# Kernel optimization log

Measured on AMD Instinct MI355X. Metric: run time of the kernel, lower is better.

## Reference

```python
import jax, jax.numpy as jnp
import numpy as np

B, IN, H = 4096, 2048, 2048

def hard_sigmoid(x):
    # torch nn.Hardsigmoid / QHardSigmoid: clip(x/6 + 0.5, 0, 1)
    return jnp.clip(x / 6.0 + 0.5, 0.0, 1.0)

def hard_tanh(x):
    return jnp.clip(x, -1.0, 1.0)

def setup_inputs() -> dict:
    key = jax.random.key(0)
    k1, k2, k3, k4, k5 = jax.random.split(key, 5)
    return {
        "input_": jax.random.normal(k1, (B, IN), dtype=jnp.float32),
        "h_0": jax.random.normal(k2, (B, H), dtype=jnp.float32),
        "c_0": jax.random.normal(k3, (B, H), dtype=jnp.float32),
        "W_ih": jax.random.normal(k4, (4 * H, IN), dtype=jnp.float32) * (1.0 / np.sqrt(IN)),
        "W_hh": jax.random.normal(k5, (4 * H, H), dtype=jnp.float32) * (1.0 / np.sqrt(H)),
        "b_hh": jnp.zeros((4 * H,), dtype=jnp.float32),
    }

def reference(input_, h_0, c_0, W_ih, W_hh, b_hh):
    # Two GEMMs: x @ W_ih^T (no bias) and h @ W_hh^T + b
    wi = jnp.einsum('bi,gi->bg', input_, W_ih)          # [B, 4H]
    wh_b = jnp.einsum('bh,gh->bg', h_0, W_hh) + b_hh     # [B, 4H]
    h_x4 = wh_b + wi
    f, i, o, g = jnp.split(h_x4, 4, axis=1)              # split order: f, i, o, g
    new = hard_sigmoid(i) * hard_tanh(g)
    old = hard_sigmoid(f) * c_0
    c_1 = old + new
    h_1 = hard_sigmoid(o) * hard_tanh(c_1)
    return (h_1, c_1)
```

## Files before the change

### kernel.cpp

```cpp
#include <hip/hip_runtime.h>
#include <hip/hip_bf16.h>


typedef __attribute__((ext_vector_type(8))) short short8;
typedef __attribute__((ext_vector_type(4))) float f32x4;

#define B_SZ 4096
#define K_SZ 4096
#define N_SZ 8192
#define H_SZ 2048

typedef const __attribute__((address_space(1))) void gvoid_t;
typedef __attribute__((address_space(3))) void lvoid_t;

__device__ __forceinline__ void gload_lds16(const __hip_bfloat16* g, void* l) {
    __builtin_amdgcn_global_load_lds((gvoid_t*)g, (lvoid_t*)l, 16, 0, 0);
}

__device__ __forceinline__ float hsig(float x) {
    return fminf(fmaxf(x * (1.0f / 6.0f) + 0.5f, 0.0f), 1.0f);
}
__device__ __forceinline__ float htanh(float x) {
    return fminf(fmaxf(x, -1.0f), 1.0f);
}

__device__ __forceinline__ void cvt8_store(const float* src, __hip_bfloat16* dst) {
    float4 v0 = *reinterpret_cast<const float4*>(src);
    float4 v1 = *reinterpret_cast<const float4*>(src + 4);
    union { __hip_bfloat16 h[8]; uint4 q; } p;
    p.h[0] = __float2bfloat16(v0.x); p.h[1] = __float2bfloat16(v0.y);
    p.h[2] = __float2bfloat16(v0.z); p.h[3] = __float2bfloat16(v0.w);
    p.h[4] = __float2bfloat16(v1.x); p.h[5] = __float2bfloat16(v1.y);
    p.h[6] = __float2bfloat16(v1.z); p.h[7] = __float2bfloat16(v1.w);
    *reinterpret_cast<uint4*>(dst) = p.q;
}

__global__ void cvt_concat_kernel(const float* __restrict__ a,
                                  const float* __restrict__ b,
                                  __hip_bfloat16* __restrict__ out,
                                  int total8)
{
    int i = blockIdx.x * blockDim.x + threadIdx.x;
    if (i >= total8) return;
    int idx = i << 3;
    int r = idx >> 12;
    int c = idx & 4095;
    const float* src = (c < 2048) ? (a + (size_t)r * 2048 + c)
                                  : (b + (size_t)r * 2048 + (c - 2048));
    cvt8_store(src, out + idx);
}

__global__ void cvt_w_perm_kernel(const float* __restrict__ wih,
                                  const float* __restrict__ whh,
                                  __hip_bfloat16* __restrict__ out,
                                  int total8)
{
    int i = blockIdx.x * blockDim.x + threadIdx.x;
    if (i >= total8) return;
    int idx = i << 3;
    int r = idx >> 12;
    int c = idx & 4095;
    int gate = (((r >> 7) & 1) << 1) | ((r >> 4) & 1);
    int j = (r & 15) | (((r >> 5) & 3) << 4) | ((r >> 8) << 6);
    int srow = gate * 2048 + j;
    const float* src = (c < 2048) ? (wih + (size_t)srow * 2048 + c)
                                  : (whh + (size_t)srow * 2048 + (c - 2048));
    cvt8_store(src, out + idx);
}

__global__ __launch_bounds__(512, 2)
void gemm_fused_kernel(const __hip_bfloat16* __restrict__ A,
                       const __hip_bfloat16* __restrict__ Bw,
                       const float* __restrict__ c0,
                       const float* __restrict__ bias,
                       float* __restrict__ out)
{
    constexpr int BK = 64;
    constexpr int NT = K_SZ / BK;
    constexpr int NWG = (B_SZ / 256) * (N_SZ / 256);
    constexpr int TILEB = 65536;

    extern __shared__ __align__(16) char lds[];

    const int tid  = threadIdx.x;
    const int wave = tid >> 6;
    const int lane = tid & 63;
    const int wrow = wave >> 2;
    const int wcol = wave & 3;
    const int fr   = lane & 15;
    const int fkq  = lane >> 4;

    int bid = blockIdx.x;
    int swz = (bid & 7) * (NWG / 8) + (bid >> 3);
    int bm = swz >> 5;
    int bn = swz & 31;

    const int rs  = tid >> 3;
    const int ch  = tid & 7;
    const int lch = ch ^ (rs & 7);
    const __hip_bfloat16* pa = A  + (size_t)(bm * 256 + rs) * K_SZ + lch * 8;
    const __hip_bfloat16* pb = Bw + (size_t)(bn * 256 + rs) * K_SZ + lch * 8;

#define STG_A(bufn, kt, srow) \
    gload_lds16(pa + (size_t)(srow) * K_SZ + (kt), (bufn) + (srow) * 128 + wave * 1024)
#define STG_B(bufn, kt, srow) \
    gload_lds16(pb + (size_t)(srow) * K_SZ + (kt), (bufn) + 32768 + (srow) * 128 + wave * 1024)

    int a_off[4], b_off[2];
#pragma unroll
    for (int mf = 0; mf < 4; ++mf) {
        int row = wrow * 64 + mf * 16 + fr;
        a_off[mf] = row * 128 + ((fkq ^ (row & 7)) << 4);
    }
#pragma unroll
    for (int nf = 0; nf < 2; ++nf) {
        int row = wcol * 32 + nf * 16 + fr;
        b_off[nf] = row * 128 + ((fkq ^ (row & 7)) << 4);
    }

    f32x4 acc[8][4];
#pragma unroll
    for (int m = 0; m < 8; ++m)
#pragma unroll
        for (int n = 0; n < 4; ++n)
            acc[m][n] = f32x4{0.f, 0.f, 0.f, 0.f};

    {
        char* b0 = lds;
        STG_A(b0, 0, 0);   STG_A(b0, 0, 64);
        STG_B(b0, 0, 0);   STG_B(b0, 0, 64);
        STG_B(b0, 0, 128); STG_B(b0, 0, 192);
        STG_A(b0, 0, 128); STG_A(b0, 0, 192);
    }
    asm volatile("s_waitcnt vmcnt(2)" ::: "memory");
    asm volatile("s_barrier" ::: "memory");

    short8 av[4][2], bv0[2][2], bv1[2][2];

#pragma unroll 1
    for (int t = 0; t < NT; ++t) {
        char* bufc = lds + (t & 1) * TILEB;
        char* bufn = lds + ((t + 1) & 1) * TILEB;
        const char* Ab = bufc;
        const char* Bb = bufc + 32768;
        const int ktn = (t + 1) * BK;
        const bool st = (t + 1 < NT);

#pragma unroll
        for (int mf = 0; mf < 4; ++mf)
#pragma unroll
            for (int ks = 0; ks < 2; ++ks)
                av[mf][ks] = *(const short8*)(Ab + (a_off[mf] ^ (ks << 6)));
#pragma unroll
        for (int nf = 0; nf < 2; ++nf)
#pragma unroll
            for (int ks = 0; ks < 2; ++ks) {
                bv0[nf][ks] = *(const short8*)(Bb + (b_off[nf] ^ (ks << 6)));
                bv1[nf][ks] = *(const short8*)(Bb + 16384 + (b_off[nf] ^ (ks << 6)));
            }
        if (st) { STG_A(bufn, ktn, 0); STG_A(bufn, ktn, 64); }
        asm volatile("s_barrier" ::: "memory");
        asm volatile("s_waitcnt lgkmcnt(0)" ::: "memory");
        __builtin_amdgcn_sched_barrier(0);
        __builtin_amdgcn_s_setprio(1);
#pragma unroll
        for (int mf = 0; mf < 4; ++mf)
#pragma unroll
            for (int nf = 0; nf < 2; ++nf)
#pragma unroll
                for (int ks = 0; ks < 2; ++ks)
                    acc[mf][nf] = __builtin_amdgcn_mfma_f32_16x16x32_bf16(av[mf][ks], bv0[nf][ks], acc[mf][nf], 0, 0, 0);
        __builtin_amdgcn_s_setprio(0);
        asm volatile("s_barrier" ::: "memory");

        if (st) { STG_B(bufn, ktn, 0); STG_B(bufn, ktn, 64); }
        asm volatile("s_barrier" ::: "memory");
        __builtin_amdgcn_s_setprio(1);
#pragma unroll
        for (int mf = 0; mf < 4; ++mf)
#pragma unroll
            for (int nf = 0; nf < 2; ++nf)
#pragma unroll
                for (int ks = 0; ks < 2; ++ks)
                    acc[mf][2 + nf] = __builtin_amdgcn_mfma_f32_16x16x32_bf16(av[mf][ks], bv1[nf][ks], acc[mf][2 + nf], 0, 0, 0);
        __builtin_amdgcn_s_setprio(0);
        if (st) asm volatile("s_waitcnt vmcnt(4)" ::: "memory");
        else    asm volatile("s_waitcnt vmcnt(0)" ::: "memory");
        asm volatile("s_barrier" ::: "memory");

#pragma unroll
        for (int mf = 0; mf < 4; ++mf)
#pragma unroll
            for (int ks = 0; ks < 2; ++ks)
                av[mf][ks] = *(const short8*)(Ab + 16384 + (a_off[mf] ^ (ks << 6)));
        if (st) { STG_B(bufn, ktn, 128); STG_B(bufn, ktn, 192); }
        asm volatile("s_barrier" ::: "memory");
        asm volatile("s_waitcnt lgkmcnt(0)" ::: "memory");
        __builtin_amdgcn_sched_barrier(0);
        __builtin_amdgcn_s_setprio(1);
#pragma unroll
        for (int mf = 0; mf < 4; ++mf)
#pragma unroll
            for (int nf = 0; nf < 2; ++nf)
#pragma unroll
                for (int ks = 0; ks < 2; ++ks)
                    acc[4 + mf][nf] = __builtin_amdgcn_mfma_f32_16x16x32_bf16(av[mf][ks], bv0[nf][ks], acc[4 + mf][nf], 0, 0, 0);
        __builtin_amdgcn_s_setprio(0);
        asm volatile("s_barrier" ::: "memory");

        if (st) { STG_A(bufn, ktn, 128); STG_A(bufn, ktn, 192); }
        asm volatile("s_barrier" ::: "memory");
        __builtin_amdgcn_s_setprio(1);
#pragma unroll
        for (int mf = 0; mf < 4; ++mf)
#pragma unroll
            for (int nf = 0; nf < 2; ++nf)
#pragma unroll
                for (int ks = 0; ks < 2; ++ks)
                    acc[4 + mf][2 + nf] = __builtin_amdgcn_mfma_f32_16x16x32_bf16(av[mf][ks], bv1[nf][ks], acc[4 + mf][2 + nf], 0, 0, 0);
        __builtin_amdgcn_s_setprio(0);
        if (st) asm volatile("s_waitcnt vmcnt(2)" ::: "memory");
        asm volatile("s_barrier" ::: "memory");
    }
#undef STG_A
#undef STG_B

    const int jj = bn * 64 + wcol * 16 + fr;
    const float bf = bias[jj];
    const float bi = bias[2048 + jj];
    const float bo = bias[4096 + jj];
    const float bg = bias[6144 + jj];
    float* h1out = out;
    float* c1out = out + (size_t)B_SZ * H_SZ;
#pragma unroll
    for (int mh = 0; mh < 2; ++mh)
#pragma unroll
        for (int mf = 0; mf < 4; ++mf) {
            const int m = mh * 4 + mf;
            const int row0 = bm * 256 + mh * 128 + wrow * 64 + mf * 16 + fkq * 4;
#pragma unroll
            for (int i = 0; i < 4; ++i) {
                int r = row0 + i;
                float c0v = c0[(size_t)r * H_SZ + jj];
                float f  = acc[m][0][i] + bf;
                float ig = acc[m][1][i] + bi;
                float o  = acc[m][2][i] + bo;
                float g  = acc[m][3][i] + bg;
                float cn = hsig(f) * c0v + hsig(ig) * htanh(g);
                h1out[(size_t)r * H_SZ + jj] = hsig(o) * htanh(cn);
                c1out[(size_t)r * H_SZ + jj] = cn;
            }
        }
}

extern "C" void kernel_launch(void* const* d_in, const int* in_sizes, int n_in,
                              void* d_out, int out_size, void* d_ws, size_t ws_size,
                              hipStream_t stream)
{
    const float* x   = (const float*)d_in[0];
    const float* h0  = (const float*)d_in[1];
    const float* c0  = (const float*)d_in[2];
    const float* Wih = (const float*)d_in[3];
    const float* Whh = (const float*)d_in[4];
    const float* bhh = (const float*)d_in[5];
    float* out = (float*)d_out;

    if (ws_size < (size_t)96 * 1024 * 1024) return;
    char* ws = (char*)d_ws;
    __hip_bfloat16* Xp = (__hip_bfloat16*)ws;
    __hip_bfloat16* Wp = (__hip_bfloat16*)(ws + (size_t)32 * 1024 * 1024);

    int t8x = B_SZ * K_SZ / 8;
    cvt_concat_kernel<<<t8x / 256, 256, 0, stream>>>(x, h0, Xp, t8x);
    int t8w = N_SZ * K_SZ / 8;
    cvt_w_perm_kernel<<<t8w / 256, 256, 0, stream>>>(Wih, Whh, Wp, t8w);

    gemm_fused_kernel<<<512, 512, 131072, stream>>>(Xp, Wp, c0, bhh, out);
}
```

Before: 467.2 us.

## Fuse fp32-to-bf16 conversion and weight permutation into GEMM tile loads

Removes the two separate conversion kernels and the bf16 workspace. The GEMM now loads fp32 activations and weights straight from global memory into registers, packs them to bf16 and writes them into the swizzled LDS layout, computing the gate permutation inline. It also merges the two MFMA half-phases per A sub-tile and drops several barriers. The intent is to avoid extra launches and the round trip through the workspace. The cost is twice the global bytes per tile (fp32 instead of bf16), conversion work repeated by every tile that reuses the same data, more register pressure, and no longer using direct global-to-LDS loads.

```diff
diff --git a/kernel.cpp b/kernel.cpp
--- a/kernel.cpp
+++ b/kernel.cpp
@@ -10,13 +10,6 @@
 #define N_SZ 8192
 #define H_SZ 2048
 
-typedef const __attribute__((address_space(1))) void gvoid_t;
-typedef __attribute__((address_space(3))) void lvoid_t;
-
-__device__ __forceinline__ void gload_lds16(const __hip_bfloat16* g, void* l) {
-    __builtin_amdgcn_global_load_lds((gvoid_t*)g, (lvoid_t*)l, 16, 0, 0);
-}
-
 __device__ __forceinline__ float hsig(float x) {
     return fminf(fmaxf(x * (1.0f / 6.0f) + 0.5f, 0.0f), 1.0f);
 }
@@ -24,53 +17,20 @@
     return fminf(fmaxf(x, -1.0f), 1.0f);
 }
 
-__device__ __forceinline__ void cvt8_store(const float* src, __hip_bfloat16* dst) {
-    float4 v0 = *reinterpret_cast<const float4*>(src);
-    float4 v1 = *reinterpret_cast<const float4*>(src + 4);
+__device__ __forceinline__ uint4 pack8(float4 lo, float4 hi) {
     union { __hip_bfloat16 h[8]; uint4 q; } p;
-    p.h[0] = __float2bfloat16(v0.x); p.h[1] = __float2bfloat16(v0.y);
-    p.h[2] = __float2bfloat16(v0.z); p.h[3] = __float2bfloat16(v0.w);
-    p.h[4] = __float2bfloat16(v1.x); p.h[5] = __float2bfloat16(v1.y);
-    p.h[6] = __float2bfloat16(v1.z); p.h[7] = __float2bfloat16(v1.w);
-    *reinterpret_cast<uint4*>(dst) = p.q;
-}
-
-__global__ void cvt_concat_kernel(const float* __restrict__ a,
-                                  const float* __restrict__ b,
-                                  __hip_bfloat16* __restrict__ out,
-                                  int total8)
-{
-    int i = blockIdx.x * blockDim.x + threadIdx.x;
-    if (i >= total8) return;
-    int idx = i << 3;
-    int r = idx >> 12;
-    int c = idx & 4095;
-    const float* src = (c < 2048) ? (a + (size_t)r * 2048 + c)
-                                  : (b + (size_t)r * 2048 + (c - 2048));
-    cvt8_store(src, out + idx);
-}
-
-__global__ void cvt_w_perm_kernel(const float* __restrict__ wih,
-                                  const float* __restrict__ whh,
-                                  __hip_bfloat16* __restrict__ out,
-                                  int total8)
-{
-    int i = blockIdx.x * blockDim.x + threadIdx.x;
-    if (i >= total8) return;
-    int idx = i << 3;
-    int r = idx >> 12;
-    int c = idx & 4095;
-    int gate = (((r >> 7) & 1) << 1) | ((r >> 4) & 1);
-    int j = (r & 15) | (((r >> 5) & 3) << 4) | ((r >> 8) << 6);
-    int srow = gate * 2048 + j;
-    const float* src = (c < 2048) ? (wih + (size_t)srow * 2048 + c)
-                                  : (whh + (size_t)srow * 2048 + (c - 2048));
-    cvt8_store(src, out + idx);
+    p.h[0] = __float2bfloat16(lo.x); p.h[1] = __float2bfloat16(lo.y);
+    p.h[2] = __float2bfloat16(lo.z); p.h[3] = __float2bfloat16(lo.w);
+    p.h[4] = __float2bfloat16(hi.x); p.h[5] = __float2bfloat16(hi.y);
+    p.h[6] = __float2bfloat16(hi.z); p.h[7] = __float2bfloat16(hi.w);
+    return p.q;
 }
 
 __global__ __launch_bounds__(512, 2)
-void gemm_fused_kernel(const __hip_bfloat16* __restrict__ A,
-                       const __hip_bfloat16* __restrict__ Bw,
+void gemm_fused_kernel(const float* __restrict__ x,
+                       const float* __restrict__ h0,
+                       const float* __restrict__ wih,
+                       const float* __restrict__ whh,
                        const float* __restrict__ c0,
                        const float* __restrict__ bias,
                        float* __restrict__ out)
@@ -95,16 +55,18 @@
     int bm = swz >> 5;
     int bn = swz & 31;
 
-    const int rs  = tid >> 3;
-    const int ch  = tid & 7;
-    const int lch = ch ^ (rs & 7);
-    const __hip_bfloat16* pa = A  + (size_t)(bm * 256 + rs) * K_SZ + lch * 8;
-    const __hip_bfloat16* pb = Bw + (size_t)(bn * 256 + rs) * K_SZ + lch * 8;
-
-#define STG_A(bufn, kt, srow) \
-    gload_lds16(pa + (size_t)(srow) * K_SZ + (kt), (bufn) + (srow) * 128 + wave * 1024)
-#define STG_B(bufn, kt, srow) \
-    gload_lds16(pb + (size_t)(srow) * K_SZ + (kt), (bufn) + 32768 + (srow) * 128 + wave * 1024)
+    const int rs = tid >> 3;
+    const int ch = tid & 7;
+    const int abase = (bm * 256 + rs) * 2048 + ch * 8;
+    int boff[4];
+#pragma unroll
+    for (int k = 0; k < 4; ++k) {
+        int br = rs + k * 64;
+        int gate = (((br >> 7) & 1) << 1) | ((br >> 4) & 1);
+        int j = (br & 15) | (((br >> 5) & 3) << 4) | (bn << 6);
+        boff[k] = (gate * 2048 + j) * 2048 + ch * 8;
+    }
+    const int adst = rs * 128 + ((ch ^ (rs & 7)) << 4);
 
     int a_off[4], b_off[2];
 #pragma unroll
@@ -125,17 +87,42 @@
         for (int n = 0; n < 4; ++n)
             acc[m][n] = f32x4{0.f, 0.f, 0.f, 0.f};
 
+    float4 aL0, aH0, aL1, aH1;
+    float4 bL0, bH0, bL1, bH1;
+
+#define LD_A(k0) { \
+    const float* p0 = As + abase + (k0) * 131072 + kc; \
+    const float* p1 = As + abase + ((k0) + 1) * 131072 + kc; \
+    aL0 = *(const float4*)(p0); aH0 = *(const float4*)(p0 + 4); \
+    aL1 = *(const float4*)(p1); aH1 = *(const float4*)(p1 + 4); }
+#define LD_B(k0) { \
+    const float* p0 = Ws + boff[k0] + kc; \
+    const float* p1 = Ws + boff[(k0) + 1] + kc; \
+    bL0 = *(const float4*)(p0); bH0 = *(const float4*)(p0 + 4); \
+    bL1 = *(const float4*)(p1); bH1 = *(const float4*)(p1 + 4); }
+#define WR_A(k0) { \
+    *(uint4*)(bufn + adst + (k0) * 8192) = pack8(aL0, aH0); \
+    *(uint4*)(bufn + adst + ((k0) + 1) * 8192) = pack8(aL1, aH1); }
+#define WR_B(k0) { \
+    *(uint4*)(bufn + 32768 + adst + (k0) * 8192) = pack8(bL0, bH0); \
+    *(uint4*)(bufn + 32768 + adst + ((k0) + 1) * 8192) = pack8(bL1, bH1); }
+
     {
-        char* b0 = lds;
-        STG_A(b0, 0, 0);   STG_A(b0, 0, 64);
-        STG_B(b0, 0, 0);   STG_B(b0, 0, 64);
-        STG_B(b0, 0, 128); STG_B(b0, 0, 192);
-        STG_A(b0, 0, 128); STG_A(b0, 0, 192);
-    }
-    asm volatile("s_waitcnt vmcnt(2)" ::: "memory");
-    asm volatile("s_barrier" ::: "memory");
-
-    short8 av[4][2], bv0[2][2], bv1[2][2];
+        char* bufn = lds;
+        const float* As = x;
+        const float* Ws = wih;
+        const int kc = 0;
+        LD_A(0); LD_B(0);
+        asm volatile("s_waitcnt vmcnt(4)" ::: "memory");
+        WR_A(0); LD_A(2);
+        asm volatile("s_waitcnt vmcnt(4)" ::: "memory");
+        WR_B(0); LD_B(2);
+        asm volatile("s_waitcnt vmcnt(4)" ::: "memory");
+        WR_A(2);
+        asm volatile("s_waitcnt vmcnt(0)" ::: "memory");
+        WR_B(2);
+        asm volatile("s_waitcnt lgkmcnt(0)" ::: "memory");
+    }
 
 #pragma unroll 1
     for (int t = 0; t < NT; ++t) {
@@ -143,9 +130,18 @@
         char* bufn = lds + ((t + 1) & 1) * TILEB;
         const char* Ab = bufc;
         const char* Bb = bufc + 32768;
-        const int ktn = (t + 1) * BK;
         const bool st = (t + 1 < NT);
-
+        const int knext = (t + 1) * BK;
+        const bool inx = knext < 2048;
+        const float* As = inx ? x : h0;
+        const float* Ws = inx ? wih : whh;
+        const int kc = knext & 2047;
+
+        asm volatile("s_barrier" ::: "memory");
+
+        if (st) { LD_A(0); LD_B(0); }
+
+        short8 av[4][2], bv0[2][2], bv1[2][2];
 #pragma unroll
         for (int mf = 0; mf < 4; ++mf)
 #pragma unroll
@@ -158,8 +154,6 @@
                 bv0[nf][ks] = *(const short8*)(Bb + (b_off[nf] ^ (ks << 6)));
                 bv1[nf][ks] = *(const short8*)(Bb + 16384 + (b_off[nf] ^ (ks << 6)));
             }
-        if (st) { STG_A(bufn, ktn, 0); STG_A(bufn, ktn, 64); }
-        asm volatile("s_barrier" ::: "memory");
         asm volatile("s_waitcnt lgkmcnt(0)" ::: "memory");
         __builtin_amdgcn_sched_barrier(0);
         __builtin_amdgcn_s_setprio(1);
@@ -168,33 +162,27 @@
 #pragma unroll
             for (int nf = 0; nf < 2; ++nf)
 #pragma unroll
-                for (int ks = 0; ks < 2; ++ks)
-                    acc[mf][nf] = __builtin_amdgcn_mfma_f32_16x16x32_bf16(av[mf][ks], bv0[nf][ks], acc[mf][nf], 0, 0, 0);
+                for (int ks = 0; ks < 2; ++ks) {
+                    acc[mf][nf]     = __builtin_amdgcn_mfma_f32_16x16x32_bf16(av[mf][ks], bv0[nf][ks], acc[mf][nf], 0, 0, 0);
+                    acc[mf][2 + nf] = __builtin_amdgcn_mfma_f32_16x16x32_bf16(av[mf][ks], bv1[nf][ks], acc[mf][2 + nf], 0, 0, 0);
+                }
         __builtin_amdgcn_s_setprio(0);
-        asm volatile("s_barrier" ::: "memory");
-
-        if (st) { STG_B(bufn, ktn, 0); STG_B(bufn, ktn, 64); }
-        asm volatile("s_barrier" ::: "memory");
-        __builtin_amdgcn_s_setprio(1);
-#pragma unroll
-        for (int mf = 0; mf < 4; ++mf)
-#pragma unroll
-            for (int nf = 0; nf < 2; ++nf)
-#pragma unroll
-                for (int ks = 0; ks < 2; ++ks)
-                    acc[mf][2 + nf] = __builtin_amdgcn_mfma_f32_16x16x32_bf16(av[mf][ks], bv1[nf][ks], acc[mf][2 + nf], 0, 0, 0);
-        __builtin_amdgcn_s_setprio(0);
-        if (st) asm volatile("s_waitcnt vmcnt(4)" ::: "memory");
-        else    asm volatile("s_waitcnt vmcnt(0)" ::: "memory");
-        asm volatile("s_barrier" ::: "memory");
-
+
+        if (st) {
+            asm volatile("s_waitcnt vmcnt(4)" ::: "memory");
+            __builtin_amdgcn_sched_barrier(0);
+            WR_A(0); LD_A(2);
+            asm volatile("s_waitcnt vmcnt(4)" ::: "memory");
+            __builtin_amdgcn_sched_barrier(0);
+            WR_B(0); LD_B(2);
+        }
+
+        short8 aw[4][2];
 #pragma unroll
         for (int mf = 0; mf < 4; ++mf)
 #pragma unroll
             for (int ks = 0; ks < 2; ++ks)
-                av[mf][ks] = *(const short8*)(Ab + 16384 + (a_off[mf] ^ (ks << 6)));
-        if (st) { STG_B(bufn, ktn, 128); STG_B(bufn, ktn, 192); }
-        asm volatile("s_barrier" ::: "memory");
+                aw[mf][ks] = *(const short8*)(Ab + 16384 + (a_off[mf] ^ (ks << 6)));
         asm volatile("s_waitcnt lgkmcnt(0)" ::: "memory");
         __builtin_amdgcn_sched_barrier(0);
         __builtin_amdgcn_s_setprio(1);
@@ -203,27 +191,26 @@
 #pragma unroll
             for (int nf = 0; nf < 2; ++nf)
 #pragma unroll
-                for (int ks = 0; ks < 2; ++ks)
-                    acc[4 + mf][nf] = __builtin_amdgcn_mfma_f32_16x16x32_bf16(av[mf][ks], bv0[nf][ks], acc[4 + mf][nf], 0, 0, 0);
+                for (int ks = 0; ks < 2; ++ks) {
+                    acc[4 + mf][nf]     = __builtin_amdgcn_mfma_f32_16x16x32_bf16(aw[mf][ks], bv0[nf][ks], acc[4 + mf][nf], 0, 0, 0);
+                    acc[4 + mf][2 + nf] = __builtin_amdgcn_mfma_f32_16x16x32_bf16(aw[mf][ks], bv1[nf][ks], acc[4 + mf][2 + nf], 0, 0, 0);
+                }
         __builtin_amdgcn_s_setprio(0);
-        asm volatile("s_barrier" ::: "memory");
-
-        if (st) { STG_A(bufn, ktn, 128); STG_A(bufn, ktn, 192); }
-        asm volatile("s_barrier" ::: "memory");
-        __builtin_amdgcn_s_setprio(1);
-#pragma unroll
-        for (int mf = 0; mf < 4; ++mf)
-#pragma unroll
-            for (int nf = 0; nf < 2; ++nf)
-#pragma unroll
-                for (int ks = 0; ks < 2; ++ks)
-                    acc[4 + mf][2 + nf] = __builtin_amdgcn_mfma_f32_16x16x32_bf16(av[mf][ks], bv1[nf][ks], acc[4 + mf][2 + nf], 0, 0, 0);
-        __builtin_amdgcn_s_setprio(0);
-        if (st) asm volatile("s_waitcnt vmcnt(2)" ::: "memory");
-        asm volatile("s_barrier" ::: "memory");
-    }
-#undef STG_A
-#undef STG_B
+
+        if (st) {
+            asm volatile("s_waitcnt vmcnt(4)" ::: "memory");
+            __builtin_amdgcn_sched_barrier(0);
+            WR_A(2);
+            asm volatile("s_waitcnt vmcnt(0)" ::: "memory");
+            __builtin_amdgcn_sched_barrier(0);
+            WR_B(2);
+            asm volatile("s_waitcnt lgkmcnt(0)" ::: "memory");
+        }
+    }
+#undef LD_A
+#undef LD_B
+#undef WR_A
+#undef WR_B
 
     const int jj = bn * 64 + wcol * 16 + fr;
     const float bf = bias[jj];
@@ -265,15 +252,5 @@
     const float* bhh = (const float*)d_in[5];
     float* out = (float*)d_out;
 
-    if (ws_size < (size_t)96 * 1024 * 1024) return;
-    char* ws = (char*)d_ws;
-    __hip_bfloat16* Xp = (__hip_bfloat16*)ws;
-    __hip_bfloat16* Wp = (__hip_bfloat16*)(ws + (size_t)32 * 1024 * 1024);
-
-    int t8x = B_SZ * K_SZ / 8;
-    cvt_concat_kernel<<<t8x / 256, 256, 0, stream>>>(x, h0, Xp, t8x);
-    int t8w = N_SZ * K_SZ / 8;
-    cvt_w_perm_kernel<<<t8w / 256, 256, 0, stream>>>(Wih, Whh, Wp, t8w);
-
-    gemm_fused_kernel<<<512, 512, 131072, stream>>>(Xp, Wp, c0, bhh, out);
-}
+    gemm_fused_kernel<<<512, 512, 131072, stream>>>(x, h0, Wih, Whh, c0, bhh, out);
+}
```

New measurement: 1.071 ms. 129% more time.

## Merge conversion kernels and restructure GEMM main loop into two phases

Applied to the files above, without the earlier changes.

Combines the two fp32-to-bf16 conversion kernels into a single grid-stride launch, removing one kernel launch. The GEMM main loop goes from four barrier-separated MFMA phases with interleaved partial tile loads to two phases. All eight global-to-LDS loads for the next tile are issued up front, and each phase now covers both B halves. This cuts the number of barriers per K-step and lengthens MFMA runs, but it issues all prefetches at once and adds an extra A register set, which may raise register pressure at 2 waves/SIMD occupancy.

```diff
diff --git a/kernel.cpp b/kernel.cpp
--- a/kernel.cpp
+++ b/kernel.cpp
@@ -35,37 +35,36 @@
     *reinterpret_cast<uint4*>(dst) = p.q;
 }
 
-__global__ void cvt_concat_kernel(const float* __restrict__ a,
-                                  const float* __restrict__ b,
-                                  __hip_bfloat16* __restrict__ out,
-                                  int total8)
+__global__ void cvt_all_kernel(const float* __restrict__ x,
+                               const float* __restrict__ h0,
+                               const float* __restrict__ wih,
+                               const float* __restrict__ whh,
+                               __hip_bfloat16* __restrict__ Xp,
+                               __hip_bfloat16* __restrict__ Wp)
 {
-    int i = blockIdx.x * blockDim.x + threadIdx.x;
-    if (i >= total8) return;
-    int idx = i << 3;
-    int r = idx >> 12;
-    int c = idx & 4095;
-    const float* src = (c < 2048) ? (a + (size_t)r * 2048 + c)
-                                  : (b + (size_t)r * 2048 + (c - 2048));
-    cvt8_store(src, out + idx);
-}
-
-__global__ void cvt_w_perm_kernel(const float* __restrict__ wih,
-                                  const float* __restrict__ whh,
-                                  __hip_bfloat16* __restrict__ out,
-                                  int total8)
-{
-    int i = blockIdx.x * blockDim.x + threadIdx.x;
-    if (i >= total8) return;
-    int idx = i << 3;
-    int r = idx >> 12;
-    int c = idx & 4095;
-    int gate = (((r >> 7) & 1) << 1) | ((r >> 4) & 1);
-    int j = (r & 15) | (((r >> 5) & 3) << 4) | ((r >> 8) << 6);
-    int srow = gate * 2048 + j;
-    const float* src = (c < 2048) ? (wih + (size_t)srow * 2048 + c)
-                                  : (whh + (size_t)srow * 2048 + (c - 2048));
-    cvt8_store(src, out + idx);
+    constexpr int XT = B_SZ * K_SZ / 8;
+    constexpr int WT = N_SZ * K_SZ / 8;
+    const int stride = gridDim.x * blockDim.x;
+    for (int i = blockIdx.x * blockDim.x + threadIdx.x; i < XT + WT; i += stride) {
+        if (i < XT) {
+            int idx = i << 3;
+            int r = idx >> 12;
+            int c = idx & 4095;
+            const float* src = (c < 2048) ? (x + (size_t)r * 2048 + c)
+                                          : (h0 + (size_t)r * 2048 + (c - 2048));
+            cvt8_store(src, Xp + idx);
+        } else {
+            int idx = (i - XT) << 3;
+            int r = idx >> 12;
+            int c = idx & 4095;
+            int gate = (((r >> 7) & 1) << 1) | ((r >> 4) & 1);
+            int j = (r & 15) | (((r >> 5) & 3) << 4) | ((r >> 8) << 6);
+            int srow = gate * 2048 + j;
+            const float* src = (c < 2048) ? (wih + (size_t)srow * 2048 + c)
+                                          : (whh + (size_t)srow * 2048 + (c - 2048));
+            cvt8_store(src, Wp + idx);
+        }
+    }
 }
 
 __global__ __launch_bounds__(512, 2)
@@ -105,6 +104,11 @@
     gload_lds16(pa + (size_t)(srow) * K_SZ + (kt), (bufn) + (srow) * 128 + wave * 1024)
 #define STG_B(bufn, kt, srow) \
     gload_lds16(pb + (size_t)(srow) * K_SZ + (kt), (bufn) + 32768 + (srow) * 128 + wave * 1024)
+#define STG_TILE(bufn, kt) { \
+    STG_A(bufn, kt, 0);   STG_A(bufn, kt, 64); \
+    STG_B(bufn, kt, 0);   STG_B(bufn, kt, 64); \
+    STG_B(bufn, kt, 128); STG_B(bufn, kt, 192); \
+    STG_A(bufn, kt, 128); STG_A(bufn, kt, 192); }
 
     int a_off[4], b_off[2];
 #pragma unroll
@@ -125,17 +129,9 @@
         for (int n = 0; n < 4; ++n)
             acc[m][n] = f32x4{0.f, 0.f, 0.f, 0.f};
 
-    {
-        char* b0 = lds;
-        STG_A(b0, 0, 0);   STG_A(b0, 0, 64);
-        STG_B(b0, 0, 0);   STG_B(b0, 0, 64);
-        STG_B(b0, 0, 128); STG_B(b0, 0, 192);
-        STG_A(b0, 0, 128); STG_A(b0, 0, 192);
-    }
+    STG_TILE(lds, 0);
     asm volatile("s_waitcnt vmcnt(2)" ::: "memory");
     asm volatile("s_barrier" ::: "memory");
-
-    short8 av[4][2], bv0[2][2], bv1[2][2];
 
 #pragma unroll 1
     for (int t = 0; t < NT; ++t) {
@@ -146,6 +142,7 @@
         const int ktn = (t + 1) * BK;
         const bool st = (t + 1 < NT);
 
+        short8 av[4][2], bv0[2][2], bv1[2][2];
 #pragma unroll
         for (int mf = 0; mf < 4; ++mf)
 #pragma unroll
@@ -158,7 +155,7 @@
                 bv0[nf][ks] = *(const short8*)(Bb + (b_off[nf] ^ (ks << 6)));
                 bv1[nf][ks] = *(const short8*)(Bb + 16384 + (b_off[nf] ^ (ks << 6)));
             }
-        if (st) { STG_A(bufn, ktn, 0); STG_A(bufn, ktn, 64); }
+        if (st) STG_TILE(bufn, ktn);
         asm volatile("s_barrier" ::: "memory");
         asm volatile("s_waitcnt lgkmcnt(0)" ::: "memory");
         __builtin_amdgcn_sched_barrier(0);
@@ -168,32 +165,21 @@
 #pragma unroll
             for (int nf = 0; nf < 2; ++nf)
 #pragma unroll
-                for (int ks = 0; ks < 2; ++ks)
-                    acc[mf][nf] = __builtin_amdgcn_mfma_f32_16x16x32_bf16(av[mf][ks], bv0[nf][ks], acc[mf][nf], 0, 0, 0);
+                for (int ks = 0; ks < 2; ++ks) {
+                    acc[mf][nf]     = __builtin_amdgcn_mfma_f32_16x16x32_bf16(av[mf][ks], bv0[nf][ks], acc[mf][nf], 0, 0, 0);
+                    acc[mf][2 + nf] = __builtin_amdgcn_mfma_f32_16x16x32_bf16(av[mf][ks], bv1[nf][ks], acc[mf][2 + nf], 0, 0, 0);
+                }
         __builtin_amdgcn_s_setprio(0);
-        asm volatile("s_barrier" ::: "memory");
-
-        if (st) { STG_B(bufn, ktn, 0); STG_B(bufn, ktn, 64); }
-        asm volatile("s_barrier" ::: "memory");
-        __builtin_amdgcn_s_setprio(1);
-#pragma unroll
-        for (int mf = 0; mf < 4; ++mf)
-#pragma unroll
-            for (int nf = 0; nf < 2; ++nf)
-#pragma unroll
-                for (int ks = 0; ks < 2; ++ks)
-                    acc[mf][2 + nf] = __builtin_amdgcn_mfma_f32_16x16x32_bf16(av[mf][ks], bv1[nf][ks], acc[mf][2 + nf], 0, 0, 0);
-        __builtin_amdgcn_s_setprio(0);
-        if (st) asm volatile("s_waitcnt vmcnt(4)" ::: "memory");
+        if (st) asm volatile("s_waitcnt vmcnt(8)" ::: "memory");
         else    asm volatile("s_waitcnt vmcnt(0)" ::: "memory");
         asm volatile("s_barrier" ::: "memory");
 
+        short8 aw[4][2];
 #pragma unroll
         for (int mf = 0; mf < 4; ++mf)
 #pragma unroll
             for (int ks = 0; ks < 2; ++ks)
-                av[mf][ks] = *(const short8*)(Ab + 16384 + (a_off[mf] ^ (ks << 6)));
-        if (st) { STG_B(bufn, ktn, 128); STG_B(bufn, ktn, 192); }
+                aw[mf][ks] = *(const short8*)(Ab + 16384 + (a_off[mf] ^ (ks << 6)));
         asm volatile("s_barrier" ::: "memory");
         asm volatile("s_waitcnt lgkmcnt(0)" ::: "memory");
         __builtin_amdgcn_sched_barrier(0);
@@ -203,27 +189,17 @@
 #pragma unroll
             for (int nf = 0; nf < 2; ++nf)
 #pragma unroll
-                for (int ks = 0; ks < 2; ++ks)
-                    acc[4 + mf][nf] = __builtin_amdgcn_mfma_f32_16x16x32_bf16(av[mf][ks], bv0[nf][ks], acc[4 + mf][nf], 0, 0, 0);
-        __builtin_amdgcn_s_setprio(0);
-        asm volatile("s_barrier" ::: "memory");
-
-        if (st) { STG_A(bufn, ktn, 128); STG_A(bufn, ktn, 192); }
-        asm volatile("s_barrier" ::: "memory");
-        __builtin_amdgcn_s_setprio(1);
-#pragma unroll
-        for (int mf = 0; mf < 4; ++mf)
-#pragma unroll
-            for (int nf = 0; nf < 2; ++nf)
-#pragma unroll
-                for (int ks = 0; ks < 2; ++ks)
-                    acc[4 + mf][2 + nf] = __builtin_amdgcn_mfma_f32_16x16x32_bf16(av[mf][ks], bv1[nf][ks], acc[4 + mf][2 + nf], 0, 0, 0);
+                for (int ks = 0; ks < 2; ++ks) {
+                    acc[4 + mf][nf]     = __builtin_amdgcn_mfma_f32_16x16x32_bf16(aw[mf][ks], bv0[nf][ks], acc[4 + mf][nf], 0, 0, 0);
+                    acc[4 + mf][2 + nf] = __builtin_amdgcn_mfma_f32_16x16x32_bf16(aw[mf][ks], bv1[nf][ks], acc[4 + mf][2 + nf], 0, 0, 0);
+                }
         __builtin_amdgcn_s_setprio(0);
         if (st) asm volatile("s_waitcnt vmcnt(2)" ::: "memory");
         asm volatile("s_barrier" ::: "memory");
     }
 #undef STG_A
 #undef STG_B
+#undef STG_TILE
 
     const int jj = bn * 64 + wcol * 16 + fr;
     const float bf = bias[jj];
@@ -270,10 +246,6 @@
     __hip_bfloat16* Xp = (__hip_bfloat16*)ws;
     __hip_bfloat16* Wp = (__hip_bfloat16*)(ws + (size_t)32 * 1024 * 1024);
 
-    int t8x = B_SZ * K_SZ / 8;
-    cvt_concat_kernel<<<t8x / 256, 256, 0, stream>>>(x, h0, Xp, t8x);
-    int t8w = N_SZ * K_SZ / 8;
-    cvt_w_perm_kernel<<<t8w / 256, 256, 0, stream>>>(Wih, Whh, Wp, t8w);
-
+    cvt_all_kernel<<<2048, 256, 0, stream>>>(x, h0, Wih, Whh, Xp, Wp);
     gemm_fused_kernel<<<512, 512, 131072, stream>>>(Xp, Wp, c0, bhh, out);
 }
```

Result: slower. 490.9 us (+5.1%).
